# Kernel optimization log

Hardware: AMD Instinct MI355X
Metric: run time of the kernel (lower is better)

Reference implementation:

```python
import jax, jax.numpy as jnp
import numpy as np

WS = 16          # window_size
NUM_HEADS = 6

def _rel_tables(ws):
    # SwinV2 continuous relative coords table, log-spaced, scaled by 8
    r = np.arange(-(ws - 1), ws, dtype=np.float32)
    t = np.stack(np.meshgrid(r, r, indexing='ij'), axis=-1)      # (2ws-1, 2ws-1, 2)
    t = t / (ws - 1) * 8.0
    t = np.sign(t) * np.log2(np.abs(t) + 1.0) / np.log2(8.0)
    c = np.stack(np.meshgrid(np.arange(ws), np.arange(ws), indexing='ij')).reshape(2, -1)
    rel = (c[:, :, None] - c[:, None, :]).transpose(1, 2, 0)     # (N, N, 2)
    rel[..., 0] += ws - 1
    rel[..., 1] += ws - 1
    rel[..., 0] *= 2 * ws - 1
    return jnp.asarray(t), jnp.asarray(rel.sum(-1))              # table, (N,N) int index

REL_TABLE, REL_INDEX = _rel_tables(WS)

def conv2d(x, w, b, pad=0, dil=1, groups=1):
    y = jax.lax.conv_general_dilated(
        x, w, (1, 1), [(pad, pad), (pad, pad)], rhs_dilation=(dil, dil),
        feature_group_count=groups, dimension_numbers=('NCHW', 'OIHW', 'NCHW'))
    return y + b[None, :, None, None]

def layernorm(x, g, b, eps=1e-5):
    mu = x.mean(-1, keepdims=True)
    var = ((x - mu) ** 2).mean(-1, keepdims=True)
    return (x - mu) * jax.lax.rsqrt(var + eps) * g + b

def _forward(x, p1_w, p1_b, pw_w, pw_b, dw_w, dw_b, dd_w, dd_b, p2_w, p2_b,
             ln_g, ln_b, qkv_w, q_bias, v_bias, logit_scale,
             cpb_w1, cpb_b1, cpb_w2, proj_w, proj_b):
    B, C, H, W = x.shape
    ws, nh = WS, NUM_HEADS
    N, hd = ws * ws, C // nh
    # ---- VAB: conv attention block ----
    y = jax.nn.gelu(conv2d(x, p1_w, p1_b), approximate=False)          # proj_1 + GELU
    a = conv2d(y, pw_w, pw_b)                                          # pointwise 1x1
    a = conv2d(a, dw_w, dw_b, pad=2, groups=C)                         # depthwise 5x5
    a = conv2d(a, dd_w, dd_b, pad=6, dil=3, groups=C)                  # depthwise 5x5 dil=3
    y = conv2d(y * a, p2_w, p2_b) + x                                  # proj_2 + residual
    y = jnp.transpose(y, (0, 2, 3, 1))                                 # B,H,W,C
    y = layernorm(y, ln_g, ln_b)                                       # pixel_norm
    # ---- window partition -> (B*nW, N, C) ----
    xw = y.reshape(B, H // ws, ws, W // ws, ws, C)
    xw = xw.transpose(0, 1, 3, 2, 4, 5).reshape(-1, N, C)
    # ---- SwinV2 cosine window attention ----
    qkv_b = jnp.concatenate([q_bias, jnp.zeros_like(v_bias), v_bias])
    qkv = (xw @ qkv_w.T + qkv_b).reshape(-1, N, 3, nh, hd).transpose(2, 0, 3, 1, 4)
    q, k, v = qkv[0], qkv[1], qkv[2]                                   # (B_, h, N, d)
    qn = q / jnp.maximum(jnp.linalg.norm(q, axis=-1, keepdims=True), 1e-12)
    kn = k / jnp.maximum(jnp.linalg.norm(k, axis=-1, keepdims=True), 1e-12)
    scale = jnp.exp(jnp.minimum(logit_scale, jnp.log(100.0)))          # clamp at 1/0.01
    attn = jnp.einsum('bhnd,bhmd->bhnm', qn, kn) * scale
    # CPB MLP bias: (2ws-1,2ws-1,2) -> heads, gathered by relative_position_index
    t = (jax.nn.relu(REL_TABLE @ cpb_w1.T + cpb_b1) @ cpb_w2.T).reshape(-1, nh)
    rpb = t[REL_INDEX.reshape(-1)].reshape(N, N, nh).transpose(2, 0, 1)
    attn = attn + 16.0 * jax.nn.sigmoid(rpb)
    attn = jax.nn.softmax(attn, axis=-1)
    out = jnp.einsum('bhnm,bhmd->bhnd', attn, v).transpose(0, 2, 1, 3).reshape(-1, N, C)
    out = out @ proj_w.T + proj_b
    # ---- window reverse -> NCHW ----
    out = out.reshape(B, H // ws, W // ws, ws, ws, C)
    out = out.transpose(0, 1, 3, 2, 4, 5).reshape(B, H, W, C)
    return jnp.transpose(out, (0, 3, 1, 2))

def setup_inputs():
    key = jax.random.key(0)
    ks = jax.random.split(key, 12)
    C, A = 192, 192
    rn = lambda k, shape, s=0.02: jax.random.normal(k, shape, jnp.float32) * s
    return {
        'x': jax.random.normal(ks[0], (4, C, 128, 128), jnp.float32),
        'p1_w': rn(ks[1], (A, C, 1, 1)), 'p1_b': jnp.zeros((A,), jnp.float32),
        'pw_w': rn(ks[2], (A, A, 1, 1)), 'pw_b': jnp.zeros((A,), jnp.float32),
        'dw_w': rn(ks[3], (A, 1, 5, 5), 0.05), 'dw_b': jnp.zeros((A,), jnp.float32),
        'dd_w': rn(ks[4], (A, 1, 5, 5), 0.05), 'dd_b': jnp.zeros((A,), jnp.float32),
        'p2_w': rn(ks[5], (C, A, 1, 1)), 'p2_b': jnp.zeros((C,), jnp.float32),
        'ln_g': jnp.ones((C,), jnp.float32), 'ln_b': jnp.zeros((C,), jnp.float32),
        'qkv_w': rn(ks[6], (3 * C, C)),
        'q_bias': jnp.zeros((C,), jnp.float32), 'v_bias': jnp.zeros((C,), jnp.float32),
        'logit_scale': jnp.log(10.0) * jnp.ones((NUM_HEADS, 1, 1), jnp.float32),
        'cpb_w1': rn(ks[7], (512, 2), 0.1), 'cpb_b1': jnp.zeros((512,), jnp.float32),
        'cpb_w2': rn(ks[8], (NUM_HEADS, 512), 0.1),
        'proj_w': rn(ks[9], (C, C)), 'proj_b': jnp.zeros((C,), jnp.float32),
    }

def reference(x, p1_w, p1_b, pw_w, pw_b, dw_w, dw_b, dd_w, dd_b, p2_w, p2_b,
              ln_g, ln_b, qkv_w, q_bias, v_bias, logit_scale,
              cpb_w1, cpb_b1, cpb_w2, proj_w, proj_b):
    return _forward(x, p1_w, p1_b, pw_w, pw_b, dw_w, dw_b, dd_w, dd_b, p2_w, p2_b,
                    ln_g, ln_b, qkv_w, q_bias, v_bias, logit_scale,
                    cpb_w1, cpb_b1, cpb_w2, proj_w, proj_b)
```

## Files before the change

kernel.cpp:

```cpp
#include <hip/hip_runtime.h>
#include <hip/hip_bf16.h>
#include <math.h>

#define HWC 16384
#define CCH 192
#define LDA 200

typedef __attribute__((ext_vector_type(8))) short short8x;
typedef __attribute__((ext_vector_type(4))) float f32x4;

__device__ __forceinline__ float b2f(unsigned int u){
  union { unsigned int i; float f; } x; x.i = (u & 0xffffu) << 16; return x.f;
}
__device__ __forceinline__ unsigned short f2b(float f){
  union { float f; unsigned int i; } x; x.f = f;
  unsigned int r = x.i + 0x7FFFu + ((x.i >> 16) & 1u);
  return (unsigned short)(r >> 16);
}
__device__ __forceinline__ float gelu_exact(float v){
  return 0.5f * v * (1.0f + erff(v * 0.70710678118654752440f));
}

__global__ __launch_bounds__(256) void cast_w_kernel(
    const float* __restrict__ qkvw, const float* __restrict__ projw,
    const float* __restrict__ p1w,  const float* __restrict__ pww,
    const float* __restrict__ p2w,  const float* __restrict__ dww,
    const float* __restrict__ ddw,
    unsigned short* __restrict__ wq,  unsigned short* __restrict__ wprj,
    unsigned short* __restrict__ wp1, unsigned short* __restrict__ wpa,
    unsigned short* __restrict__ wp2, float* __restrict__ dwt,
    float* __restrict__ ddt)
{
  int i = blockIdx.x*256 + threadIdx.x;
  if (i < 110592) wq[i] = f2b(qkvw[i]);
  if (i < 36864){
    wprj[i] = f2b(projw[i]);
    wp1[i]  = f2b(p1w[i]);
    wpa[i]  = f2b(pww[i]);
    wp2[i]  = f2b(p2w[i]);
  }
  if (i < 4800){
    int t = i / 192, c = i - t*192;
    dwt[i] = dww[c*25 + t];
    ddt[i] = ddw[c*25 + t];
  }
}

__global__ __launch_bounds__(256) void tx_kernel(
    const float* __restrict__ in, float* __restrict__ xt32,
    unsigned short* __restrict__ x16)
{
  __shared__ float xs[CCH*68];
  const int tid = threadIdx.x;
  const int pix0 = blockIdx.x * 64;
  const int bb = pix0 >> 14;
  const int hw0 = pix0 & (HWC-1);
  const long base = (long)bb * CCH * HWC + hw0;
  #pragma unroll 8
  for (int i=0;i<48;i++){
    int idx = tid + i*256;
    int ci = idx >> 6, pix = idx & 63;
    xs[ci*68 + pix] = in[base + (long)ci*HWC + pix];
  }
  __syncthreads();
  #pragma unroll 8
  for (int i=0;i<48;i++){
    int idx = tid + i*256;
    int pix = idx / 192, ci = idx - pix*192;
    float v = xs[ci*68 + pix];
    long g = (long)(pix0 + pix)*CCH + ci;
    xt32[g] = v;
    x16[g]  = f2b(v);
  }
}

template<int MODE>
__global__ __launch_bounds__(256, 3) void pw_mfma(
    const unsigned short* __restrict__ in0,
    const unsigned short* __restrict__ in1,
    const unsigned short* __restrict__ w16,
    const float* __restrict__ bias,
    const float* __restrict__ xres,
    const float* __restrict__ gam, const float* __restrict__ bet,
    unsigned short* __restrict__ out16)
{
  __shared__ unsigned short sA[128*LDA];
  __shared__ float reds[128*2], reds2[128*2];
  const int tid = threadIdx.x;
  const int m0 = blockIdx.x * 128;
  #pragma unroll
  for (int i=0;i<12;i++){
    int idx = tid + i*256;
    int row = idx / 24, oct = idx - row*24;
    long g = (long)(m0+row)*CCH + oct*8;
    uint4 vy = *(const uint4*)(in0 + g);
    if (MODE == 2){
      uint4 va = *(const uint4*)(in1 + g);
      unsigned int yy[4] = {vy.x, vy.y, vy.z, vy.w};
      unsigned int aa[4] = {va.x, va.y, va.z, va.w};
      unsigned int rr[4];
      #pragma unroll
      for (int wq2=0; wq2<4; wq2++){
        float lo = b2f(yy[wq2]) * b2f(aa[wq2]);
        float hi = b2f(yy[wq2] >> 16) * b2f(aa[wq2] >> 16);
        rr[wq2] = (unsigned int)f2b(lo) | ((unsigned int)f2b(hi) << 16);
      }
      uint4 vp; vp.x=rr[0]; vp.y=rr[1]; vp.z=rr[2]; vp.w=rr[3];
      *(uint4*)&sA[row*LDA + oct*8] = vp;
    } else {
      *(uint4*)&sA[row*LDA + oct*8] = vy;
    }
  }
  __syncthreads();
  const int wv = tid >> 6, lane = tid & 63;
  const int wm = (wv & 1) * 64;
  const int wn = (wv >> 1) * 96;
  const int l15 = lane & 15, q = lane >> 4;
  f32x4 acc[4][6];
  #pragma unroll
  for (int mi=0;mi<4;mi++)
    #pragma unroll
    for (int ni=0;ni<6;ni++) acc[mi][ni] = (f32x4){0.f,0.f,0.f,0.f};
  #pragma unroll
  for (int kk=0; kk<6; kk++){
    const int k0 = kk*32;
    short8x af[4], bf[6];
    #pragma unroll
    for (int mi=0; mi<4; mi++)
      af[mi] = *(const short8x*)&sA[(wm + mi*16 + l15)*LDA + k0 + q*8];
    #pragma unroll
    for (int ni=0; ni<6; ni++)
      bf[ni] = *(const short8x*)(w16 + (long)(wn + ni*16 + l15)*CCH + k0 + q*8);
    #pragma unroll
    for (int mi=0; mi<4; mi++)
      #pragma unroll
      for (int ni=0; ni<6; ni++)
        acc[mi][ni] = __builtin_amdgcn_mfma_f32_16x16x32_bf16(af[mi], bf[ni], acc[mi][ni], 0,0,0);
  }
  float bv[6];
  #pragma unroll
  for (int ni=0; ni<6; ni++) bv[ni] = bias[wn + ni*16 + l15];

  if (MODE != 2){
    #pragma unroll
    for (int mi=0; mi<4; mi++){
      #pragma unroll
      for (int r=0; r<4; r++){
        long gp = (long)(m0 + wm + mi*16 + q*4 + r)*CCH + wn;
        #pragma unroll
        for (int ni=0; ni<6; ni++){
          float v = acc[mi][ni][r] + bv[ni];
          if (MODE == 0) v = gelu_exact(v);
          out16[gp + ni*16 + l15] = f2b(v);
        }
      }
    }
  } else {
    const int slot = wv >> 1;
    #pragma unroll
    for (int mi=0; mi<4; mi++){
      #pragma unroll
      for (int r=0; r<4; r++){
        int pixl = wm + mi*16 + q*4 + r;
        long gp = (long)(m0 + pixl)*CCH + wn;
        float s = 0.f, s2 = 0.f;
        #pragma unroll
        for (int ni=0; ni<6; ni++){
          float v = acc[mi][ni][r] + bv[ni] + xres[gp + ni*16 + l15];
          acc[mi][ni][r] = v;
          s += v; s2 = fmaf(v, v, s2);
        }
        s  += __shfl_xor(s, 1);  s  += __shfl_xor(s, 2);
        s  += __shfl_xor(s, 4);  s  += __shfl_xor(s, 8);
        s2 += __shfl_xor(s2, 1); s2 += __shfl_xor(s2, 2);
        s2 += __shfl_xor(s2, 4); s2 += __shfl_xor(s2, 8);
        if (l15 == 0){ reds[pixl*2 + slot] = s; reds2[pixl*2 + slot] = s2; }
      }
    }
    __syncthreads();
    #pragma unroll
    for (int mi=0; mi<4; mi++){
      #pragma unroll
      for (int r=0; r<4; r++){
        int pixl = wm + mi*16 + q*4 + r;
        long gp = (long)(m0 + pixl)*CCH + wn;
        float st  = reds[pixl*2] + reds[pixl*2+1];
        float s2t = reds2[pixl*2] + reds2[pixl*2+1];
        float mu = st * (1.0f/192.0f);
        float var = s2t * (1.0f/192.0f) - mu*mu;
        float rs = rsqrtf(var + 1e-5f);
        #pragma unroll
        for (int ni=0; ni<6; ni++){
          int co = wn + ni*16 + l15;
          float z = (acc[mi][ni][r] - mu) * rs * gam[co] + bet[co];
          out16[gp + ni*16 + l15] = f2b(z);
        }
      }
    }
  }
}

template<int PAD, int DIL>
__global__ __launch_bounds__(256) void dw_nhwc(
    const unsigned short* __restrict__ in16, const float* __restrict__ wT,
    const float* __restrict__ bias, unsigned short* __restrict__ out16)
{
  const int g = blockIdx.x;
  const int wid = (g & 7) * 768 + (g >> 3);
  const int t = wid*256 + threadIdx.x;
  const int c8 = t % 24, pix = t / 24;
  const int row = (pix >> 7) & 127, col = pix & 127;
  const int c0 = c8 * 8;
  const long ibase = (long)(pix & ~(HWC-1)) * CCH;
  float acc[8];
  {
    float4 b0 = *(const float4*)&bias[c0], b1 = *(const float4*)&bias[c0+4];
    acc[0]=b0.x; acc[1]=b0.y; acc[2]=b0.z; acc[3]=b0.w;
    acc[4]=b1.x; acc[5]=b1.y; acc[6]=b1.z; acc[7]=b1.w;
  }
  #pragma unroll
  for (int kh=0; kh<5; kh++){
    int ih = row + kh*DIL - PAD;
    if ((unsigned)ih < 128u){
      #pragma unroll
      for (int kw=0; kw<5; kw++){
        int iw = col + kw*DIL - PAD;
        if ((unsigned)iw < 128u){
          uint4 v = *(const uint4*)(in16 + ibase + (long)(ih*128 + iw)*CCH + c0);
          const float* wp = wT + (kh*5 + kw)*CCH + c0;
          float4 w0 = *(const float4*)wp, w1 = *(const float4*)(wp + 4);
          unsigned int uu[4] = {v.x, v.y, v.z, v.w};
          float wa[8] = {w0.x, w0.y, w0.z, w0.w, w1.x, w1.y, w1.z, w1.w};
          #pragma unroll
          for (int j=0; j<8; j++){
            float xv = b2f(uu[j>>1] >> ((j&1)*16));
            acc[j] = fmaf(wa[j], xv, acc[j]);
          }
        }
      }
    }
  }
  unsigned int rr[4];
  #pragma unroll
  for (int wq2=0; wq2<4; wq2++)
    rr[wq2] = (unsigned int)f2b(acc[wq2*2]) | ((unsigned int)f2b(acc[wq2*2+1]) << 16);
  uint4 o; o.x=rr[0]; o.y=rr[1]; o.z=rr[2]; o.w=rr[3];
  *(uint4*)(out16 + (long)pix*CCH + c0) = o;
}

__global__ __launch_bounds__(256, 3) void qkv_fused(
    const unsigned short* __restrict__ z16,
    const unsigned short* __restrict__ w16,
    const float* __restrict__ qb, const float* __restrict__ vb,
    const float* __restrict__ ls,
    unsigned short* __restrict__ qkvb)
{
  __shared__ unsigned short sA[128*LDA];
  const int tid = threadIdx.x;
  const int m0 = blockIdx.x * 128;
  const int s  = blockIdx.y;
  #pragma unroll
  for (int i=0;i<12;i++){
    int idx = tid + i*256;
    int row = idx / 24, oct = idx - row*24;
    uint4 v = *(const uint4*)(z16 + (long)(m0+row)*CCH + oct*8);
    *(uint4*)&sA[row*LDA + oct*8] = v;
  }
  __syncthreads();
  const int wv = tid >> 6, lane = tid & 63;
  const int wm = (wv & 1) * 64;
  const int wn = (wv >> 1) * 96;
  const int l15 = lane & 15, q = lane >> 4;
  const unsigned short* wbase = w16 + (long)(s*192)*CCH;
  f32x4 acc[4][6];
  #pragma unroll
  for (int mi=0;mi<4;mi++)
    #pragma unroll
    for (int ni=0;ni<6;ni++) acc[mi][ni] = (f32x4){0.f,0.f,0.f,0.f};
  #pragma unroll
  for (int kk=0; kk<6; kk++){
    const int k0 = kk*32;
    short8x af[4], bf[6];
    #pragma unroll
    for (int mi=0; mi<4; mi++)
      af[mi] = *(const short8x*)&sA[(wm + mi*16 + l15)*LDA + k0 + q*8];
    #pragma unroll
    for (int ni=0; ni<6; ni++)
      bf[ni] = *(const short8x*)(wbase + (long)(wn + ni*16 + l15)*CCH + k0 + q*8);
    #pragma unroll
    for (int mi=0; mi<4; mi++)
      #pragma unroll
      for (int ni=0; ni<6; ni++)
        acc[mi][ni] = __builtin_amdgcn_mfma_f32_16x16x32_bf16(af[mi], bf[ni], acc[mi][ni], 0,0,0);
  }
  float bvv[6];
  #pragma unroll
  for (int ni=0;ni<6;ni++){
    int co = wn + ni*16 + l15;
    bvv[ni] = (s==0) ? qb[co] : ((s==2) ? vb[co] : 0.0f);
  }
  float sc_[3] = {1.f, 1.f, 1.f};
  if (s == 0){
    #pragma unroll
    for (int hp=0;hp<3;hp++)
      sc_[hp] = __expf(fminf(ls[(wn>>5)+hp], 4.60517018598809136804f));
  }
  unsigned short* dst = qkvb + (long)s * 12582912;
  const int head0 = wn >> 5;
  #pragma unroll
  for (int mi=0; mi<4; mi++){
    #pragma unroll
    for (int r=0; r<4; r++){
      int pix = m0 + wm + mi*16 + q*4 + r;
      int hw = pix & (HWC-1);
      int win = (pix>>14)*64 + ((hw>>11)&7)*8 + ((hw>>4)&7);
      int tok = ((hw>>7)&15)*16 + (hw&15);
      long ob = (long)win*49152 + (long)tok*32;
      float vv[6];
      #pragma unroll
      for (int ni=0;ni<6;ni++) vv[ni] = acc[mi][ni][r] + bvv[ni];
      if (s != 2){
        float s0 = vv[0]*vv[0] + vv[1]*vv[1];
        float s1 = vv[2]*vv[2] + vv[3]*vv[3];
        float s2 = vv[4]*vv[4] + vv[5]*vv[5];
        #pragma unroll
        for (int xm=1; xm<16; xm<<=1){
          s0 += __shfl_xor(s0, xm);
          s1 += __shfl_xor(s1, xm);
          s2 += __shfl_xor(s2, xm);
        }
        float i0 = sc_[0]/fmaxf(sqrtf(s0),1e-12f);
        float i1 = sc_[1]/fmaxf(sqrtf(s1),1e-12f);
        float i2 = sc_[2]/fmaxf(sqrtf(s2),1e-12f);
        vv[0]*=i0; vv[1]*=i0; vv[2]*=i1; vv[3]*=i1; vv[4]*=i2; vv[5]*=i2;
      }
      #pragma unroll
      for (int ni=0;ni<6;ni++)
        dst[ob + (long)(head0 + (ni>>1))*8192 + (ni&1)*16 + l15] = f2b(vv[ni]);
    }
  }
}

__device__ __forceinline__ float cpb_coord(int a){
  float r = ((float)a - 15.0f) * (8.0f/15.0f);
  float t = log2f(fabsf(r) + 1.0f) * (1.0f/3.0f);
  return (r < 0.f) ? -t : t;
}
__global__ __launch_bounds__(128) void cpb_mlp_kernel(
    const float* __restrict__ w1, const float* __restrict__ b1,
    const float* __restrict__ w2, float* __restrict__ tbl6)
{
  int e = blockIdx.x;
  int a = e / 31, bb = e - a*31;
  float t0 = cpb_coord(a), t1 = cpb_coord(bb);
  float p[6] = {0,0,0,0,0,0};
  for (int hh = threadIdx.x; hh < 512; hh += 128){
    float hid = t0*w1[hh*2] + t1*w1[hh*2+1] + b1[hh];
    hid = fmaxf(hid, 0.0f);
    #pragma unroll
    for (int hd=0; hd<6; hd++) p[hd] = fmaf(hid, w2[hd*512 + hh], p[hd]);
  }
  __shared__ float red[6][128];
  #pragma unroll
  for (int hd=0; hd<6; hd++) red[hd][threadIdx.x] = p[hd];
  __syncthreads();
  if (threadIdx.x < 6){
    float sum = 0.f;
    for (int i=0;i<128;i++) sum += red[threadIdx.x][i];
    tbl6[e*6 + threadIdx.x] = sum;
  }
}
__global__ __launch_bounds__(256) void cpb_expand_kernel(
    const float* __restrict__ tbl6, float* __restrict__ bias)
{
  int idx = blockIdx.x*256 + threadIdx.x;
  int h = idx >> 16;
  int rem = idx & 65535;
  int i = rem >> 8, j = rem & 255;
  int dy = (i>>4) - (j>>4) + 15;
  int dx = (i&15) - (j&15) + 15;
  float v = tbl6[(dy*31+dx)*6 + h];
  bias[idx] = 16.0f / (1.0f + __expf(-v)) - 16.0f;
}

#define KSP 40
#define VTP 264
__global__ __launch_bounds__(256) void attn_mfma(
    const unsigned short* __restrict__ qkvb, const float* __restrict__ bias,
    unsigned short* __restrict__ aout)
{
  __shared__ unsigned short ks[256*KSP];
  __shared__ unsigned short vt[32*VTP];
  __shared__ unsigned short ps[4][64*KSP];
  const int win = blockIdx.x, h = blockIdx.y;
  const int t = threadIdx.x;
  const long base = ((long)(win*6 + h)) << 13;
  const unsigned short* Qg = qkvb + base;
  const unsigned short* Kg = Qg + 12582912;
  const unsigned short* Vg = Kg + 12582912;

  {
    const unsigned short* kr = Kg + t*32;
    uint4 k0v = *(const uint4*)(kr+0);
    uint4 k1v = *(const uint4*)(kr+8);
    uint4 k2v = *(const uint4*)(kr+16);
    uint4 k3v = *(const uint4*)(kr+24);
    *(uint4*)&ks[t*KSP +  0] = k0v;
    *(uint4*)&ks[t*KSP +  8] = k1v;
    *(uint4*)&ks[t*KSP + 16] = k2v;
    *(uint4*)&ks[t*KSP + 24] = k3v;
    union { unsigned short u[32]; uint4 v4[4]; } vp;
    const unsigned short* vr = Vg + t*32;
    #pragma unroll
    for (int o=0;o<4;o++) vp.v4[o] = *(const uint4*)(vr + o*8);
    #pragma unroll
    for (int d=0; d<32; d++) vt[d*VTP + t] = vp.u[d];
  }
  const int wv = t >> 6, lane = t & 63;
  const int l15 = lane & 15, q = lane >> 4;
  short8x qa[4];
  #pragma unroll
  for (int mi=0; mi<4; mi++)
    qa[mi] = *(const short8x*)(Qg + (wv*64 + mi*16 + l15)*32 + q*8);
  __syncthreads();

  f32x4 oacc[4][2], lsum[4];
  #pragma unroll
  for (int mi=0;mi<4;mi++){
    oacc[mi][0] = (f32x4){0.f,0.f,0.f,0.f};
    oacc[mi][1] = (f32x4){0.f,0.f,0.f,0.f};
    lsum[mi]    = (f32x4){0.f,0.f,0.f,0.f};
  }
  const float* bias_h = bias + (h << 16);
  unsigned short* myps = ps[wv];

  for (int kt=0; kt<8; kt++){
    const int k0 = kt*32;
    short8x kb0 = *(const short8x*)&ks[(k0 + l15)*KSP + q*8];
    short8x kb1 = *(const short8x*)&ks[(k0 + 16 + l15)*KSP + q*8];
    f32x4 s[4][2];
    __builtin_amdgcn_s_setprio(1);
    #pragma unroll
    for (int mi=0; mi<4; mi++){
      f32x4 z0 = (f32x4){0.f,0.f,0.f,0.f};
      s[mi][0] = __builtin_amdgcn_mfma_f32_16x16x32_bf16(qa[mi], kb0, z0, 0,0,0);
      s[mi][1] = __builtin_amdgcn_mfma_f32_16x16x32_bf16(qa[mi], kb1, z0, 0,0,0);
    }
    __builtin_amdgcn_s_setprio(0);
    #pragma unroll
    for (int mi=0; mi<4; mi++){
      #pragma unroll
      for (int r=0; r<4; r++){
        int rowq = wv*64 + mi*16 + q*4 + r;
        const float* brow = bias_h + rowq*256 + k0;
        float e0 = __expf(fminf(s[mi][0][r] + brow[l15],      30.f));
        float e1 = __expf(fminf(s[mi][1][r] + brow[16 + l15], 30.f));
        lsum[mi][r] += e0 + e1;
        myps[(mi*16 + q*4 + r)*KSP + l15]      = f2b(e0);
        myps[(mi*16 + q*4 + r)*KSP + 16 + l15] = f2b(e1);
      }
    }
    short8x vb0 = *(const short8x*)&vt[(l15)*VTP      + k0 + q*8];
    short8x vb1 = *(const short8x*)&vt[(16 + l15)*VTP + k0 + q*8];
    __builtin_amdgcn_s_setprio(1);
    #pragma unroll
    for (int mi=0; mi<4; mi++){
      short8x pa = *(const short8x*)&myps[(mi*16 + l15)*KSP + q*8];
      oacc[mi][0] = __builtin_amdgcn_mfma_f32_16x16x32_bf16(pa, vb0, oacc[mi][0], 0,0,0);
      oacc[mi][1] = __builtin_amdgcn_mfma_f32_16x16x32_bf16(pa, vb1, oacc[mi][1], 0,0,0);
    }
    __builtin_amdgcn_s_setprio(0);
  }
  #pragma unroll
  for (int mi=0; mi<4; mi++){
    #pragma unroll
    for (int r=0; r<4; r++){
      float v = lsum[mi][r];
      v += __shfl_xor(v, 1);
      v += __shfl_xor(v, 2);
      v += __shfl_xor(v, 4);
      v += __shfl_xor(v, 8);
      lsum[mi][r] = v;
    }
  }
  const int bb = win >> 6, wy = (win >> 3) & 7, wx = win & 7;
  #pragma unroll
  for (int mi=0; mi<4; mi++){
    #pragma unroll
    for (int r=0; r<4; r++){
      int rowq = wv*64 + mi*16 + q*4 + r;
      int pixo = bb*HWC + (wy*16 + (rowq>>4))*128 + wx*16 + (rowq&15);
      float inv = 1.0f / lsum[mi][r];
      aout[(long)pixo*CCH + h*32 + l15]      = f2b(oacc[mi][0][r]*inv);
      aout[(long)pixo*CCH + h*32 + 16 + l15] = f2b(oacc[mi][1][r]*inv);
    }
  }
}

__global__ __launch_bounds__(256, 3) void proj_mfma(
    const unsigned short* __restrict__ a16,
    const unsigned short* __restrict__ w16,
    const float* __restrict__ bias,
    float* __restrict__ outp)
{
  __shared__ unsigned short sB[128*LDA];
  const int tid = threadIdx.x;
  const int n0 = blockIdx.x * 128;
  #pragma unroll
  for (int i=0;i<12;i++){
    int idx = tid + i*256;
    int row = idx / 24, oct = idx - row*24;
    uint4 v = *(const uint4*)(a16 + (long)(n0+row)*CCH + oct*8);
    *(uint4*)&sB[row*LDA + oct*8] = v;
  }
  __syncthreads();
  const int wv = tid >> 6, lane = tid & 63;
  const int wm = (wv & 1) * 96;
  const int wn = (wv >> 1) * 64;
  const int l15 = lane & 15, q = lane >> 4;
  f32x4 acc[6][4];
  #pragma unroll
  for (int mi=0;mi<6;mi++)
    #pragma unroll
    for (int ni=0;ni<4;ni++) acc[mi][ni] = (f32x4){0.f,0.f,0.f,0.f};
  #pragma unroll
  for (int kk=0; kk<6; kk++){
    const int k0 = kk*32;
    short8x af[6], bf[4];
    #pragma unroll
    for (int mi=0; mi<6; mi++)
      af[mi] = *(const short8x*)(w16 + (long)(wm + mi*16 + l15)*CCH + k0 + q*8);
    #pragma unroll
    for (int ni=0; ni<4; ni++)
      bf[ni] = *(const short8x*)&sB[(wn + ni*16 + l15)*LDA + k0 + q*8];
    #pragma unroll
    for (int mi=0; mi<6; mi++)
      #pragma unroll
      for (int ni=0; ni<4; ni++)
        acc[mi][ni] = __builtin_amdgcn_mfma_f32_16x16x32_bf16(af[mi], bf[ni], acc[mi][ni], 0,0,0);
  }
  #pragma unroll
  for (int mi=0; mi<6; mi++){
    #pragma unroll
    for (int r=0; r<4; r++){
      int co = wm + mi*16 + q*4 + r;
      float bv = bias[co];
      #pragma unroll
      for (int ni=0; ni<4; ni++){
        int pix = n0 + wn + ni*16 + l15;
        int b = pix >> 14, hw = pix & (HWC-1);
        outp[((long)b*CCH + co)*HWC + hw] = acc[mi][ni][r] + bv;
      }
    }
  }
}

extern "C" void kernel_launch(void* const* d_in, const int* in_sizes, int n_in,
                              void* d_out, int out_size, void* d_ws, size_t ws_size,
                              hipStream_t stream)
{
  const float* x       = (const float*)d_in[0];
  const float* p1_w    = (const float*)d_in[1];
  const float* p1_b    = (const float*)d_in[2];
  const float* pw_w    = (const float*)d_in[3];
  const float* pw_b    = (const float*)d_in[4];
  const float* dw_w    = (const float*)d_in[5];
  const float* dw_b    = (const float*)d_in[6];
  const float* dd_w    = (const float*)d_in[7];
  const float* dd_b    = (const float*)d_in[8];
  const float* p2_w    = (const float*)d_in[9];
  const float* p2_b    = (const float*)d_in[10];
  const float* ln_g    = (const float*)d_in[11];
  const float* ln_b    = (const float*)d_in[12];
  const float* qkv_w   = (const float*)d_in[13];
  const float* q_bias  = (const float*)d_in[14];
  const float* v_bias  = (const float*)d_in[15];
  const float* lscale  = (const float*)d_in[16];
  const float* cpb_w1  = (const float*)d_in[17];
  const float* cpb_b1  = (const float*)d_in[18];
  const float* cpb_w2  = (const float*)d_in[19];
  const float* proj_w  = (const float*)d_in[20];
  const float* proj_b  = (const float*)d_in[21];

  float* ws = (float*)d_ws;
  const long A = 12582912L;
  unsigned short* X16  = (unsigned short*)ws;
  unsigned short* Y16  = (unsigned short*)(ws + A/2);
  unsigned short* A16  = (unsigned short*)(ws + A);
  unsigned short* T16  = (unsigned short*)(ws + A + A/2);
  float* XT32 = ws + 2*A;
  unsigned short* QKVB = (unsigned short*)ws;
  unsigned short* Z16  = (unsigned short*)(ws + 3*A);
  unsigned short* AO16 = Z16;
  float* DWT = ws + 3*A + A/2;
  float* DDT = DWT + 4800;
  unsigned short* WQ   = (unsigned short*)(DDT + 4800);
  unsigned short* WPRJ = WQ + 110592;
  unsigned short* WP1  = WPRJ + 36864;
  unsigned short* WPA  = WP1 + 36864;
  unsigned short* WP2  = WPA + 36864;
  float* RB = ws + 4*A;
  float* T6 = RB + 393216;

  cast_w_kernel<<<432, 256, 0, stream>>>(qkv_w, proj_w, p1_w, pw_w, p2_w, dw_w, dd_w,
                                         WQ, WPRJ, WP1, WPA, WP2, DWT, DDT);
  cpb_mlp_kernel<<<961, 128, 0, stream>>>(cpb_w1, cpb_b1, cpb_w2, T6);
  cpb_expand_kernel<<<1536, 256, 0, stream>>>(T6, RB);

  tx_kernel<<<1024, 256, 0, stream>>>(x, XT32, X16);

  pw_mfma<0><<<512, 256, 0, stream>>>(X16, nullptr, WP1, p1_b, nullptr, nullptr, nullptr, Y16);
  pw_mfma<1><<<512, 256, 0, stream>>>(Y16, nullptr, WPA, pw_b, nullptr, nullptr, nullptr, A16);
  dw_nhwc<2,1><<<6144, 256, 0, stream>>>(A16, DWT, dw_b, T16);
  dw_nhwc<6,3><<<6144, 256, 0, stream>>>(T16, DDT, dd_b, A16);
  pw_mfma<2><<<512, 256, 0, stream>>>(Y16, A16, WP2, p2_b, XT32, ln_g, ln_b, Z16);

  qkv_fused<<<dim3(512, 3), 256, 0, stream>>>(Z16, WQ, q_bias, v_bias, lscale, QKVB);

  attn_mfma<<<dim3(256, 6), 256, 0, stream>>>(QKVB, RB, AO16);

  proj_mfma<<<512, 256, 0, stream>>>(AO16, WPRJ, proj_b, (float*)d_out);
}
```

Measured before the change: 503.9 us.

## Fuse Q/K/V projections per block and defer cosine normalization into attention

```diff
diff --git a/kernel.cpp b/kernel.cpp
--- a/kernel.cpp
+++ b/kernel.cpp
@@ -252,13 +252,11 @@
     const unsigned short* __restrict__ z16,
     const unsigned short* __restrict__ w16,
     const float* __restrict__ qb, const float* __restrict__ vb,
-    const float* __restrict__ ls,
     unsigned short* __restrict__ qkvb)
 {
   __shared__ unsigned short sA[128*LDA];
   const int tid = threadIdx.x;
   const int m0 = blockIdx.x * 128;
-  const int s  = blockIdx.y;
   #pragma unroll
   for (int i=0;i<12;i++){
     int idx = tid + i*256;
@@ -271,72 +269,60 @@
   const int wm = (wv & 1) * 64;
   const int wn = (wv >> 1) * 96;
   const int l15 = lane & 15, q = lane >> 4;
-  const unsigned short* wbase = w16 + (long)(s*192)*CCH;
-  f32x4 acc[4][6];
-  #pragma unroll
-  for (int mi=0;mi<4;mi++)
-    #pragma unroll
-    for (int ni=0;ni<6;ni++) acc[mi][ni] = (f32x4){0.f,0.f,0.f,0.f};
-  #pragma unroll
-  for (int kk=0; kk<6; kk++){
-    const int k0 = kk*32;
-    short8x af[4], bf[6];
-    #pragma unroll
-    for (int mi=0; mi<4; mi++)
-      af[mi] = *(const short8x*)&sA[(wm + mi*16 + l15)*LDA + k0 + q*8];
-    #pragma unroll
-    for (int ni=0; ni<6; ni++)
-      bf[ni] = *(const short8x*)(wbase + (long)(wn + ni*16 + l15)*CCH + k0 + q*8);
-    #pragma unroll
-    for (int mi=0; mi<4; mi++)
+  const int head0 = wn >> 5;
+  int winm[4], tokb[4];
+  #pragma unroll
+  for (int mi=0;mi<4;mi++){
+    int pb = m0 + wm + mi*16;
+    int hw = pb & (HWC-1);
+    int row = hw >> 7, col = hw & 127;
+    winm[mi] = (pb>>14)*64 + (row>>4)*8 + (col>>4);
+    tokb[mi] = (row & 15) * 16;
+  }
+  #pragma unroll
+  for (int s=0; s<3; s++){
+    const unsigned short* wbase = w16 + (long)(s*192)*CCH;
+    f32x4 acc[4][6];
+    #pragma unroll
+    for (int mi=0;mi<4;mi++)
+      #pragma unroll
+      for (int ni=0;ni<6;ni++) acc[mi][ni] = (f32x4){0.f,0.f,0.f,0.f};
+    #pragma unroll
+    for (int kk=0; kk<6; kk++){
+      const int k0 = kk*32;
+      short8x af[4], bf[6];
+      #pragma unroll
+      for (int mi=0; mi<4; mi++)
+        af[mi] = *(const short8x*)&sA[(wm + mi*16 + l15)*LDA + k0 + q*8];
       #pragma unroll
       for (int ni=0; ni<6; ni++)
-        acc[mi][ni] = __builtin_amdgcn_mfma_f32_16x16x32_bf16(af[mi], bf[ni], acc[mi][ni], 0,0,0);
-  }
-  float bvv[6];
-  #pragma unroll
-  for (int ni=0;ni<6;ni++){
-    int co = wn + ni*16 + l15;
-    bvv[ni] = (s==0) ? qb[co] : ((s==2) ? vb[co] : 0.0f);
-  }
-  float sc_[3] = {1.f, 1.f, 1.f};
-  if (s == 0){
-    #pragma unroll
-    for (int hp=0;hp<3;hp++)
-      sc_[hp] = __expf(fminf(ls[(wn>>5)+hp], 4.60517018598809136804f));
-  }
-  unsigned short* dst = qkvb + (long)s * 12582912;
-  const int head0 = wn >> 5;
-  #pragma unroll
-  for (int mi=0; mi<4; mi++){
-    #pragma unroll
-    for (int r=0; r<4; r++){
-      int pix = m0 + wm + mi*16 + q*4 + r;
-      int hw = pix & (HWC-1);
-      int win = (pix>>14)*64 + ((hw>>11)&7)*8 + ((hw>>4)&7);
-      int tok = ((hw>>7)&15)*16 + (hw&15);
-      long ob = (long)win*49152 + (long)tok*32;
-      float vv[6];
-      #pragma unroll
-      for (int ni=0;ni<6;ni++) vv[ni] = acc[mi][ni][r] + bvv[ni];
-      if (s != 2){
-        float s0 = vv[0]*vv[0] + vv[1]*vv[1];
-        float s1 = vv[2]*vv[2] + vv[3]*vv[3];
-        float s2 = vv[4]*vv[4] + vv[5]*vv[5];
+        bf[ni] = *(const short8x*)(wbase + (long)(wn + ni*16 + l15)*CCH + k0 + q*8);
+      #pragma unroll
+      for (int mi=0; mi<4; mi++)
         #pragma unroll
-        for (int xm=1; xm<16; xm<<=1){
-          s0 += __shfl_xor(s0, xm);
-          s1 += __shfl_xor(s1, xm);
-          s2 += __shfl_xor(s2, xm);
+        for (int ni=0; ni<6; ni++)
+          acc[mi][ni] = __builtin_amdgcn_mfma_f32_16x16x32_bf16(af[mi], bf[ni], acc[mi][ni], 0,0,0);
+    }
+    float bvv[6];
+    #pragma unroll
+    for (int ni=0;ni<6;ni++){
+      int co = wn + ni*16 + l15;
+      bvv[ni] = (s==0) ? qb[co] : ((s==2) ? vb[co] : 0.0f);
+    }
+    unsigned short* dst = qkvb + (long)s * 12582912;
+    #pragma unroll
+    for (int mi=0; mi<4; mi++){
+      long obase = (long)winm[mi]*49152 + (long)tokb[mi]*32 + l15*2;
+      #pragma unroll
+      for (int r=0; r<4; r++){
+        long ob = obase + (q*4 + r)*32;
+        #pragma unroll
+        for (int hp=0; hp<3; hp++){
+          unsigned int u = (unsigned int)f2b(acc[mi][hp*2][r]   + bvv[hp*2])
+                         | ((unsigned int)f2b(acc[mi][hp*2+1][r] + bvv[hp*2+1]) << 16);
+          *(unsigned int*)&dst[ob + (long)(head0 + hp)*8192] = u;
         }
-        float i0 = sc_[0]/fmaxf(sqrtf(s0),1e-12f);
-        float i1 = sc_[1]/fmaxf(sqrtf(s1),1e-12f);
-        float i2 = sc_[2]/fmaxf(sqrtf(s2),1e-12f);
-        vv[0]*=i0; vv[1]*=i0; vv[2]*=i1; vv[3]*=i1; vv[4]*=i2; vv[5]*=i2;
-      }
-      #pragma unroll
-      for (int ni=0;ni<6;ni++)
-        dst[ob + (long)(head0 + (ni>>1))*8192 + (ni&1)*16 + l15] = f2b(vv[ni]);
+      }
     }
   }
 }
@@ -387,34 +373,63 @@
 #define VTP 264
 __global__ __launch_bounds__(256) void attn_mfma(
     const unsigned short* __restrict__ qkvb, const float* __restrict__ bias,
+    const float* __restrict__ ls,
     unsigned short* __restrict__ aout)
 {
   __shared__ unsigned short ks[256*KSP];
   __shared__ unsigned short vt[32*VTP];
   __shared__ unsigned short ps[4][64*KSP];
+  __shared__ float qinvs[256], kinvs[256];
   const int win = blockIdx.x, h = blockIdx.y;
   const int t = threadIdx.x;
   const long base = ((long)(win*6 + h)) << 13;
   const unsigned short* Qg = qkvb + base;
   const unsigned short* Kg = Qg + 12582912;
   const unsigned short* Vg = Kg + 12582912;
+  const float sc = __expf(fminf(ls[h], 4.60517018598809136804f));
 
   {
     const unsigned short* kr = Kg + t*32;
-    uint4 k0v = *(const uint4*)(kr+0);
-    uint4 k1v = *(const uint4*)(kr+8);
-    uint4 k2v = *(const uint4*)(kr+16);
-    uint4 k3v = *(const uint4*)(kr+24);
-    *(uint4*)&ks[t*KSP +  0] = k0v;
-    *(uint4*)&ks[t*KSP +  8] = k1v;
-    *(uint4*)&ks[t*KSP + 16] = k2v;
-    *(uint4*)&ks[t*KSP + 24] = k3v;
+    uint4 kv[4];
+    #pragma unroll
+    for (int o=0;o<4;o++) kv[o] = *(const uint4*)(kr + o*8);
+    #pragma unroll
+    for (int o=0;o<4;o++) *(uint4*)&ks[t*KSP + o*8] = kv[o];
+    float sk = 0.f;
+    #pragma unroll
+    for (int o=0;o<4;o++){
+      unsigned int uu[4] = {kv[o].x, kv[o].y, kv[o].z, kv[o].w};
+      #pragma unroll
+      for (int j=0;j<4;j++){
+        float lo = b2f(uu[j]), hi = b2f(uu[j]>>16);
+        sk = fmaf(lo, lo, sk); sk = fmaf(hi, hi, sk);
+      }
+    }
+    float sq = 0.f;
+    const unsigned short* qr = Qg + t*32;
+    #pragma unroll
+    for (int o=0;o<4;o++){
+      uint4 qv = *(const uint4*)(qr + o*8);
+      unsigned int uu[4] = {qv.x, qv.y, qv.z, qv.w};
+      #pragma unroll
+      for (int j=0;j<4;j++){
+        float lo = b2f(uu[j]), hi = b2f(uu[j]>>16);
+        sq = fmaf(lo, lo, sq); sq = fmaf(hi, hi, sq);
+      }
+    }
+    kinvs[t] = 1.0f / fmaxf(sqrtf(sk), 1e-12f);
+    qinvs[t] = sc   / fmaxf(sqrtf(sq), 1e-12f);
+  }
+  {
+    const int d = t & 31, kt = t >> 5;
     union { unsigned short u[32]; uint4 v4[4]; } vp;
-    const unsigned short* vr = Vg + t*32;
-    #pragma unroll
-    for (int o=0;o<4;o++) vp.v4[o] = *(const uint4*)(vr + o*8);
-    #pragma unroll
-    for (int d=0; d<32; d++) vt[d*VTP + t] = vp.u[d];
+    #pragma unroll 4
+    for (int i=0;i<32;i++){
+      int key = kt*32 + i;
+      vp.u[i] = Vg[key*32 + d];
+    }
+    #pragma unroll
+    for (int o=0;o<4;o++) *(uint4*)&vt[d*VTP + kt*32 + o*8] = vp.v4[o];
   }
   const int wv = t >> 6, lane = t & 63;
   const int l15 = lane & 15, q = lane >> 4;
@@ -423,6 +438,11 @@
   for (int mi=0; mi<4; mi++)
     qa[mi] = *(const short8x*)(Qg + (wv*64 + mi*16 + l15)*32 + q*8);
   __syncthreads();
+
+  float4 qiv[4];
+  #pragma unroll
+  for (int mi=0; mi<4; mi++)
+    qiv[mi] = *(const float4*)&qinvs[wv*64 + mi*16 + q*4];
 
   f32x4 oacc[4][2], lsum[4];
   #pragma unroll
@@ -438,6 +458,8 @@
     const int k0 = kt*32;
     short8x kb0 = *(const short8x*)&ks[(k0 + l15)*KSP + q*8];
     short8x kb1 = *(const short8x*)&ks[(k0 + 16 + l15)*KSP + q*8];
+    const float kA = kinvs[k0 + l15];
+    const float kB = kinvs[k0 + 16 + l15];
     f32x4 s[4][2];
     __builtin_amdgcn_s_setprio(1);
     #pragma unroll
@@ -449,12 +471,14 @@
     __builtin_amdgcn_s_setprio(0);
     #pragma unroll
     for (int mi=0; mi<4; mi++){
+      const float* qivp = (const float*)&qiv[mi];
       #pragma unroll
       for (int r=0; r<4; r++){
         int rowq = wv*64 + mi*16 + q*4 + r;
         const float* brow = bias_h + rowq*256 + k0;
-        float e0 = __expf(fminf(s[mi][0][r] + brow[l15],      30.f));
-        float e1 = __expf(fminf(s[mi][1][r] + brow[16 + l15], 30.f));
+        float qr_ = qivp[r];
+        float e0 = __expf(fminf(fmaf(s[mi][0][r], qr_*kA, brow[l15]),      30.f));
+        float e1 = __expf(fminf(fmaf(s[mi][1][r], qr_*kB, brow[16 + l15]), 30.f));
         lsum[mi][r] += e0 + e1;
         myps[(mi*16 + q*4 + r)*KSP + l15]      = f2b(e0);
         myps[(mi*16 + q*4 + r)*KSP + 16 + l15] = f2b(e1);
@@ -483,6 +507,7 @@
       lsum[mi][r] = v;
     }
   }
+  const int dperm = (l15 >> 1) + ((l15 & 1) << 4);
   const int bb = win >> 6, wy = (win >> 3) & 7, wx = win & 7;
   #pragma unroll
   for (int mi=0; mi<4; mi++){
@@ -491,8 +516,8 @@
       int rowq = wv*64 + mi*16 + q*4 + r;
       int pixo = bb*HWC + (wy*16 + (rowq>>4))*128 + wx*16 + (rowq&15);
       float inv = 1.0f / lsum[mi][r];
-      aout[(long)pixo*CCH + h*32 + l15]      = f2b(oacc[mi][0][r]*inv);
-      aout[(long)pixo*CCH + h*32 + 16 + l15] = f2b(oacc[mi][1][r]*inv);
+      aout[(long)pixo*CCH + h*32 + dperm]     = f2b(oacc[mi][0][r]*inv);
+      aout[(long)pixo*CCH + h*32 + dperm + 8] = f2b(oacc[mi][1][r]*inv);
     }
   }
 }
@@ -615,9 +640,9 @@
   dw_nhwc<6,3><<<6144, 256, 0, stream>>>(T16, DDT, dd_b, A16);
   pw_mfma<2><<<512, 256, 0, stream>>>(Y16, A16, WP2, p2_b, XT32, ln_g, ln_b, Z16);
 
-  qkv_fused<<<dim3(512, 3), 256, 0, stream>>>(Z16, WQ, q_bias, v_bias, lscale, QKVB);
-
-  attn_mfma<<<dim3(256, 6), 256, 0, stream>>>(QKVB, RB, AO16);
+  qkv_fused<<<512, 256, 0, stream>>>(Z16, WQ, q_bias, v_bias, QKVB);
+
+  attn_mfma<<<dim3(256, 6), 256, 0, stream>>>(QKVB, RB, lscale, AO16);
 
   proj_mfma<<<512, 256, 0, stream>>>(AO16, WPRJ, proj_b, (float*)d_out);
 }
```

New measurement: 498.2 us. Within noise of the previous version (-1.1%).
